# Kernel tuning notes

Hardware: AMD Instinct MI355X
Metric: run time of the kernel (lower is better)

The kernel has to match this reference:

```python
import jax, jax.numpy as jnp
import numpy as np
import math

T = 4096
HID = 2048
H = 16
D = 128
RD = 64            # rotary_dim = head_dim * partial_rotary_factor (0.5)
THETA = 10000.0
EPS = 1e-6
GROUPS = 8
LAYER_IDX = 2
N_LAYERS = 32


def build_slope_tensor(num_heads):
    def get_slopes_power_of_2(n):
        start = 2 ** (-(2 ** (-(math.log2(n) - 3))))
        ratio = start
        return [start * ratio ** i for i in range(n)]
    if math.log2(num_heads).is_integer():
        return get_slopes_power_of_2(num_heads)
    closest = 2 ** math.floor(math.log2(num_heads))
    return (get_slopes_power_of_2(closest)
            + build_slope_tensor(2 * closest)[0::2][: num_heads - closest])


def compute_slope():
    base = np.array(build_slope_tensor(H), dtype=np.float32)
    return jnp.asarray(-base * (1 - (LAYER_IDX - 1) / (N_LAYERS - 1) + 1e-5), dtype=jnp.float32)


def setup_inputs() -> dict:
    key = jax.random.key(0)
    ks = jax.random.split(key, 8)
    s = 0.02
    return {
        "positions": jnp.arange(T, dtype=jnp.int32),
        "hidden_states": jax.random.normal(ks[0], (T, HID), dtype=jnp.float32),
        "recurrent_state": jnp.zeros((1, H, D, D), dtype=jnp.float32),
        "w_qkv": jax.random.normal(ks[1], (HID, 3 * H * D), dtype=jnp.float32) * s,
        "w_g": jax.random.normal(ks[2], (HID, H * D), dtype=jnp.float32) * s,
        "w_dense": jax.random.normal(ks[3], (H * D, HID), dtype=jnp.float32) * s,
        "q_norm_w": jnp.ones((D,), dtype=jnp.float32),
        "k_norm_w": jnp.ones((D,), dtype=jnp.float32),
        "g_norm_w": jnp.ones((H * D,), dtype=jnp.float32),
    }


def _rms(x, w):
    var = jnp.mean(jnp.square(x), axis=-1, keepdims=True)
    return x * jax.lax.rsqrt(var + EPS) * w


def _rope(x, positions):
    # partial neox-style rotary on first RD dims of each head
    inv_freq = 1.0 / (THETA ** (jnp.arange(0, RD, 2, dtype=jnp.float32) / RD))
    freqs = positions.astype(jnp.float32)[:, None] * inv_freq   # [T, RD/2]
    cos = jnp.cos(freqs)[:, None, :]                            # [T, 1, RD/2]
    sin = jnp.sin(freqs)[:, None, :]
    x1 = x[..., : RD // 2]
    x2 = x[..., RD // 2 : RD]
    x_pass = x[..., RD:]
    return jnp.concatenate([x1 * cos - x2 * sin, x2 * cos + x1 * sin, x_pass], axis=-1)


def reference(positions, hidden_states, recurrent_state,
              w_qkv, w_g, w_dense, q_norm_w, k_norm_w, g_norm_w):
    t = hidden_states.shape[0]
    qkv = (hidden_states @ w_qkv).reshape(t, 3, H, D)
    q, k, v = qkv[:, 0], qkv[:, 1], qkv[:, 2]
    q = _rms(q, q_norm_w)
    k = _rms(k, k_norm_w)
    q = _rope(q, positions)
    k = _rope(k, positions)

    slope = compute_slope()                    # [H], negative
    decay = jnp.exp(slope)                     # per-head per-step decay
    scale = D ** -0.5
    q = (q * scale).astype(jnp.float32)
    k = k.astype(jnp.float32)
    v = v.astype(jnp.float32)

    def step(S, qkv_t):
        q_t, k_t, v_t = qkv_t                  # each [H, D]
        S = S * decay[:, None, None] + k_t[:, :, None] * v_t[:, None, :]
        o_t = jnp.einsum('hk,hkv->hv', q_t, S)
        return S, o_t

    S0 = recurrent_state[0].astype(jnp.float32)   # [H, K, V]
    S_final, o = jax.lax.scan(step, S0, (q, k, v))
    attn = o.reshape(t, H * D)

    gate = jax.nn.sigmoid(hidden_states @ w_g)
    # GroupRMSNorm: normalize per group of size (H*D)/GROUPS, scale by full weight
    g = attn.reshape(t, GROUPS, (H * D) // GROUPS)
    var = jnp.mean(jnp.square(g), axis=-1, keepdims=True)
    g = (g * jax.lax.rsqrt(var + EPS)).reshape(t, H * D) * g_norm_w

    out = (g * gate) @ w_dense
    return out, S_final[None]
```

## Files before the change

kernel.cpp:

```cpp
#include <hip/hip_runtime.h>
#include <hip/hip_bf16.h>

using bf16x8 = __attribute__((ext_vector_type(8))) __bf16;
using f32x4  = __attribute__((ext_vector_type(4))) float;

constexpr int T_SEQ = 4096;
constexpr int HID_C = 2048;
constexpr int NH    = 16;
constexpr int QKV_N = 6144;

__device__ __forceinline__ float head_slope(int h) {
    return -exp2f(-0.5f * (float)(h + 1)) * 0.967751935483871f;
}

__device__ __forceinline__ ushort f2bfu(float f) {
    __hip_bfloat16 h = __float2bfloat16(f);
    return *(ushort*)&h;
}
__device__ __forceinline__ float bfu2f(ushort u) {
    union { unsigned int i; float f; } x; x.i = ((unsigned int)u) << 16; return x.f;
}

__device__ __forceinline__ void async16(const ushort* g, ushort* l) {
    __builtin_amdgcn_global_load_lds((const __attribute__((address_space(1))) void*)g,
                                     (__attribute__((address_space(3))) void*)l, 16, 0, 0);
}

template<int N> __device__ __forceinline__ void waitcnt_vm() {
    if constexpr (N == 0)      asm volatile("s_waitcnt vmcnt(0)" ::: "memory");
    else if constexpr (N == 2) asm volatile("s_waitcnt vmcnt(2)" ::: "memory");
    else if constexpr (N == 4) asm volatile("s_waitcnt vmcnt(4)" ::: "memory");
    else if constexpr (N == 6) asm volatile("s_waitcnt vmcnt(6)" ::: "memory");
}

__device__ __forceinline__ void cvt_body(const float* __restrict__ src, ushort* __restrict__ dst,
                                         int bid, int tid) {
    int i = (bid * 256 + tid) * 8;
    float4 a = *(const float4*)(src + i);
    float4 b = *(const float4*)(src + i + 4);
    ushort4 ua = {f2bfu(a.x), f2bfu(a.y), f2bfu(a.z), f2bfu(a.w)};
    ushort4 ub = {f2bfu(b.x), f2bfu(b.y), f2bfu(b.z), f2bfu(b.w)};
    *(ushort4*)(dst + i) = ua;
    *(ushort4*)(dst + i + 4) = ub;
}

__device__ __forceinline__ void transpose_body(const float* __restrict__ src,
                                               ushort* __restrict__ dst,
                                               int R, int C, int bx, int by, int t,
                                               ushort (*tile)[68]) {
    int tr = by * 64, tc = bx * 64;
    int r0 = t >> 4;
    int c4 = (t & 15) << 2;
#pragma unroll
    for (int p = 0; p < 4; ++p) {
        int row = r0 + p * 16;
        float4 v = *(const float4*)&src[(size_t)(tr + row) * C + tc + c4];
        tile[row][c4 + 0] = f2bfu(v.x);
        tile[row][c4 + 1] = f2bfu(v.y);
        tile[row][c4 + 2] = f2bfu(v.z);
        tile[row][c4 + 3] = f2bfu(v.w);
    }
    __syncthreads();
#pragma unroll
    for (int p = 0; p < 4; ++p) {
        int orow = r0 + p * 16;
        ushort4 u;
        u.x = tile[c4 + 0][orow];
        u.y = tile[c4 + 1][orow];
        u.z = tile[c4 + 2][orow];
        u.w = tile[c4 + 3][orow];
        *(ushort4*)&dst[(size_t)(tc + orow) * R + tr + c4] = u;
    }
}

__global__ __launch_bounds__(256) void prep_all(const float* __restrict__ hidden,
                                                ushort* __restrict__ hid_b,
                                                const float* __restrict__ w_qkv,
                                                ushort* __restrict__ wqkv_t,
                                                const float* __restrict__ w_g,
                                                ushort* __restrict__ wg_t,
                                                const float* __restrict__ w_dense,
                                                ushort* __restrict__ wd_t,
                                                const int* __restrict__ positions,
                                                float2* __restrict__ ropet) {
    __shared__ ushort tile[64][68];
    int b = blockIdx.x, t = threadIdx.x;
    if (b < 4096) {
        cvt_body(hidden, hid_b, b, t);
    } else if (b < 7168) {
        int bb = b - 4096;
        transpose_body(w_qkv, wqkv_t, HID_C, QKV_N, bb % 96, bb / 96, t, tile);
    } else if (b < 8192) {
        int bb = b - 7168;
        transpose_body(w_g, wg_t, HID_C, HID_C, bb % 32, bb / 32, t, tile);
    } else if (b < 9216) {
        int bb = b - 8192;
        transpose_body(w_dense, wd_t, HID_C, HID_C, bb % 32, bb / 32, t, tile);
    } else {
        int i = (b - 9216) * 256 + t;
        int tt = i >> 5, fi = i & 31;
        float inv = expf((float)fi * -0.2878231366f);
        float freq = (float)positions[tt] * inv;
        float sn, cs;
        sincosf(freq, &sn, &cs);
        ropet[i] = make_float2(cs, sn);
    }
}

template<int MI, int BN>
__device__ __forceinline__ void gemm8_core(const ushort* __restrict__ Ag,
                                           const ushort* __restrict__ Bg,
                                           int K, int bm, int bn,
                                           ushort* sh, f32x4 (&acc)[MI][4]) {
    constexpr int WM = 16 / MI;
    constexpr int WN = 8 / WM;
    constexpr int SB = BN / 128;
    constexpr int AH = (MI >= 8) ? 2 : 1;
    constexpr int MH = MI / AH;

    const int tid  = threadIdx.x;
    const int lane = tid & 63;
    const int wave = tid >> 6;
    const int lane15 = lane & 15, quad = lane >> 4;
    const int wm = wave / WN, wn = wave % WN;
    const int swz = lane15 & 7;

    ushort* const ldsA0 = sh;
    ushort* const ldsA1 = sh + 16384;
    ushort* const ldsB0 = sh + 32768;
    ushort* const ldsB1 = sh + 32768 + BN * 64;

    const int srow = lane >> 3;
    const int scol = ((lane & 7) ^ srow) << 3;
    const ushort* gA = Ag + (size_t)(bm + srow) * K + scol;
    const ushort* gB = Bg + (size_t)(bn + srow) * K + scol;
    const int ro  = wave * 16;
    const int roB = wave * 8 * SB;
    const int NT = K >> 6;

#define STAGE_A(L, k0) do { \
    _Pragma("unroll") for (int h = 0; h < 2; ++h) \
    _Pragma("unroll") for (int q = 0; q < 2; ++q) \
        async16(gA + (size_t)((h) * 128 + ro + q * 8) * K + (k0), (L) + ((h) * 128 + ro + q * 8) * 64); } while (0)
#define STAGE_B(L, k0) do { \
    _Pragma("unroll") for (int h = 0; h < 2; ++h) \
    _Pragma("unroll") for (int q = 0; q < SB; ++q) \
        async16(gB + (size_t)((h) * (BN / 2) + roB + q * 8) * K + (k0), (L) + ((h) * (BN / 2) + roB + q * 8) * 64); } while (0)

    STAGE_A(ldsA0, 0);
    STAGE_B(ldsB0, 0);
    waitcnt_vm<0>();
    asm volatile("s_barrier" ::: "memory");

    for (int t = 0; t < NT; ++t) {
        const ushort* LA = (t & 1) ? ldsA1 : ldsA0;
        const ushort* LB = (t & 1) ? ldsB1 : ldsB0;
        ushort* LAn = (t & 1) ? ldsA0 : ldsA1;
        ushort* LBn = (t & 1) ? ldsB0 : ldsB1;
        bf16x8 bfr[4][2];
#pragma unroll
        for (int j = 0; j < 4; ++j)
#pragma unroll
            for (int ks = 0; ks < 2; ++ks)
                bfr[j][ks] = *(const bf16x8*)&LB[(wn * 64 + j * 16 + lane15) * 64 + (((ks * 4 + quad) ^ swz) << 3)];
        bf16x8 af0[MH][2];
#pragma unroll
        for (int i = 0; i < MH; ++i)
#pragma unroll
            for (int ks = 0; ks < 2; ++ks)
                af0[i][ks] = *(const bf16x8*)&LA[(wm * (MI * 16) + i * 16 + lane15) * 64 + (((ks * 4 + quad) ^ swz) << 3)];
        if (t + 1 < NT) {
            STAGE_A(LAn, (t + 1) << 6);
            STAGE_B(LBn, (t + 1) << 6);
        }
        __builtin_amdgcn_s_setprio(1);
#pragma unroll
        for (int i = 0; i < MH; ++i)
#pragma unroll
            for (int j = 0; j < 4; ++j)
#pragma unroll
                for (int ks = 0; ks < 2; ++ks)
                    acc[i][j] = __builtin_amdgcn_mfma_f32_16x16x32_bf16(af0[i][ks], bfr[j][ks], acc[i][j], 0, 0, 0);
        __builtin_amdgcn_s_setprio(0);
        if constexpr (AH == 2) {
            bf16x8 af1[MH][2];
#pragma unroll
            for (int i = 0; i < MH; ++i)
#pragma unroll
                for (int ks = 0; ks < 2; ++ks)
                    af1[i][ks] = *(const bf16x8*)&LA[(wm * (MI * 16) + (MH + i) * 16 + lane15) * 64 + (((ks * 4 + quad) ^ swz) << 3)];
            __builtin_amdgcn_s_setprio(1);
#pragma unroll
            for (int i = 0; i < MH; ++i)
#pragma unroll
                for (int j = 0; j < 4; ++j)
#pragma unroll
                    for (int ks = 0; ks < 2; ++ks)
                        acc[MH + i][j] = __builtin_amdgcn_mfma_f32_16x16x32_bf16(af1[i][ks], bfr[j][ks], acc[MH + i][j], 0, 0, 0);
            __builtin_amdgcn_s_setprio(0);
        }
        waitcnt_vm<0>();
        asm volatile("s_barrier" ::: "memory");
    }
#undef STAGE_A
#undef STAGE_B
}

__device__ __forceinline__ void gemm4_core(const ushort* __restrict__ Ag,
                                           const ushort* __restrict__ Bg,
                                           int K, int bm, int bn,
                                           ushort* sh, f32x4 (&acc)[4][4]) {
    const int tid  = threadIdx.x;
    const int lane = tid & 63;
    const int wave = tid >> 6;
    const int lane15 = lane & 15, quad = lane >> 4;
    const int wm = wave >> 1, wn = wave & 1;
    const int swz = lane15 & 7;

    ushort* const ldsA0 = sh;
    ushort* const ldsA1 = sh + 8192;
    ushort* const ldsB0 = sh + 16384;
    ushort* const ldsB1 = sh + 24576;

    const int srow = lane >> 3;
    const int scol = ((lane & 7) ^ srow) << 3;
    const ushort* gA = Ag + (size_t)(bm + srow) * K + scol;
    const ushort* gB = Bg + (size_t)(bn + srow) * K + scol;
    const int ro = wave * 32;
    const int NT = K >> 6;

#define STG(L, g, k0) do { \
    _Pragma("unroll") for (int q = 0; q < 4; ++q) \
        async16((g) + (size_t)(ro + q * 8) * K + (k0), (L) + (ro + q * 8) * 64); } while (0)

    STG(ldsA0, gA, 0);
    STG(ldsB0, gB, 0);
    waitcnt_vm<0>();
    asm volatile("s_barrier" ::: "memory");

    for (int t = 0; t < NT; ++t) {
        const ushort* LA = (t & 1) ? ldsA1 : ldsA0;
        const ushort* LB = (t & 1) ? ldsB1 : ldsB0;
        ushort* LAn = (t & 1) ? ldsA0 : ldsA1;
        ushort* LBn = (t & 1) ? ldsB0 : ldsB1;
        bf16x8 bfr[4][2];
#pragma unroll
        for (int j = 0; j < 4; ++j)
#pragma unroll
            for (int ks = 0; ks < 2; ++ks)
                bfr[j][ks] = *(const bf16x8*)&LB[(wn * 64 + j * 16 + lane15) * 64 + (((ks * 4 + quad) ^ swz) << 3)];
        bf16x8 af[4][2];
#pragma unroll
        for (int i = 0; i < 4; ++i)
#pragma unroll
            for (int ks = 0; ks < 2; ++ks)
                af[i][ks] = *(const bf16x8*)&LA[(wm * 64 + i * 16 + lane15) * 64 + (((ks * 4 + quad) ^ swz) << 3)];
        if (t + 1 < NT) {
            STG(LAn, gA, (t + 1) << 6);
            STG(LBn, gB, (t + 1) << 6);
        }
        __builtin_amdgcn_s_setprio(1);
#pragma unroll
        for (int i = 0; i < 4; ++i)
#pragma unroll
            for (int j = 0; j < 4; ++j)
#pragma unroll
                for (int ks = 0; ks < 2; ++ks)
                    acc[i][j] = __builtin_amdgcn_mfma_f32_16x16x32_bf16(af[i][ks], bfr[j][ks], acc[i][j], 0, 0, 0);
        __builtin_amdgcn_s_setprio(0);
        waitcnt_vm<0>();
        asm volatile("s_barrier" ::: "memory");
    }
#undef STG
}

__global__ __launch_bounds__(512, 2) void gemm_fused(const ushort* __restrict__ A,
                                                     const ushort* __restrict__ Bcat,
                                                     ushort* __restrict__ qkv,
                                                     ushort* __restrict__ gate,
                                                     ushort* __restrict__ kT,
                                                     ushort* __restrict__ vT,
                                                     const float2* __restrict__ tab,
                                                     const float* __restrict__ qw,
                                                     const float* __restrict__ kw, int K) {
    __shared__ ushort sh[65536];
    int bid = blockIdx.x;
    int x = bid & 7, w = bid >> 3;
    int rm = x >> 2, rn = x & 3;
    int wm_i = w >> 3, wn_i = w & 7;
    int bm = (rm * 8 + wm_i) * 256;
    int bn = (rn * 8 + wn_i) * 256;
    f32x4 acc[8][4] = {};
    gemm8_core<8, 256>(A, Bcat, K, bm, bn, sh, acc);

    int lane = threadIdx.x & 63, wave = threadIdx.x >> 6;
    int lane15 = lane & 15, quad = lane >> 4;
    int wm = wave >> 2, wn = wave & 3;
    constexpr int S = 132;

    if (bn < 4096) {
        bool isq = bn < 2048;
        const float* wnorm = isq ? qw : kw;
        int hq = wn >> 1, dl = (wn & 1) * 64;
        int rowbase = bm + wm * 128;
        float w4[4];
#pragma unroll
        for (int j = 0; j < 4; ++j) w4[j] = wnorm[dl + j * 16 + lane15];
        float* ssb = (float*)&sh[63488];
#pragma unroll
        for (int i = 0; i < 8; ++i)
#pragma unroll
            for (int r = 0; r < 4; ++r) {
                float s2 = 0.f;
#pragma unroll
                for (int j = 0; j < 4; ++j) { float xv = acc[i][j][r]; s2 += xv * xv; }
                s2 += __shfl_xor(s2, 1);
                s2 += __shfl_xor(s2, 2);
                s2 += __shfl_xor(s2, 4);
                s2 += __shfl_xor(s2, 8);
                if (lane15 == 0) ssb[wave * 128 + i * 16 + quad * 4 + r] = s2;
            }
        __syncthreads();
        float sc = isq ? 0.08838834764831845f : 1.0f;
#pragma unroll
        for (int i = 0; i < 8; ++i)
#pragma unroll
            for (int r = 0; r < 4; ++r) {
                int row = i * 16 + quad * 4 + r;
                float ssf = ssb[wave * 128 + row] + ssb[(wave ^ 1) * 128 + row];
                float rr = rsqrtf(ssf * (1.0f / 128.0f) + 1e-6f);
                float xx[4];
#pragma unroll
                for (int j = 0; j < 4; ++j) xx[j] = acc[i][j][r] * rr * w4[j];
                if (dl == 0) {
                    int t = rowbase + row;
                    float2 rt0 = tab[t * 32 + lane15];
                    float2 rt1 = tab[t * 32 + 16 + lane15];
                    float a0 = xx[0], b0 = xx[2], a1 = xx[1], b1 = xx[3];
                    xx[0] = a0 * rt0.x - b0 * rt0.y;
                    xx[2] = b0 * rt0.x + a0 * rt0.y;
                    xx[1] = a1 * rt1.x - b1 * rt1.y;
                    xx[3] = b1 * rt1.x + a1 * rt1.y;
                }
#pragma unroll
                for (int j = 0; j < 4; ++j) acc[i][j][r] = xx[j] * sc;
            }
#pragma unroll
        for (int i = 0; i < 8; ++i)
#pragma unroll
            for (int j = 0; j < 4; ++j) {
                int col = bn + wn * 64 + j * 16 + lane15;
#pragma unroll
                for (int r = 0; r < 4; ++r)
                    qkv[(size_t)(rowbase + i * 16 + quad * 4 + r) * QKV_N + col] = f2bfu(acc[i][j][r]);
            }
        if (!isq) {
            ushort* L = sh;
            int h0 = (bn - 2048) >> 7;
            int c0 = bm >> 7;
            __syncthreads();
#pragma unroll
            for (int cq = 0; cq < 2; ++cq) {
                if (wm == cq) {
#pragma unroll
                    for (int i = 0; i < 8; ++i)
#pragma unroll
                        for (int j = 0; j < 4; ++j) {
                            int d_local = dl + j * 16 + lane15;
#pragma unroll
                            for (int r = 0; r < 4; ++r)
                                L[hq * 128 * S + d_local * S + i * 16 + quad * 4 + r] = f2bfu(acc[i][j][r]);
                        }
                }
                __syncthreads();
#pragma unroll
                for (int p = 0; p < 16; ++p) {
                    int lin = (p * 512 + threadIdx.x) * 4;
                    int hq2 = lin >> 14;
                    int wi = lin & 16383;
                    int d = wi >> 7, t4 = wi & 127;
                    const ushort* lp = &L[hq2 * 128 * S + d * S + t4];
                    ushort4 u = { lp[0], lp[1], lp[2], lp[3] };
                    *(ushort4*)&kT[((size_t)((h0 + hq2) * 32 + c0 + cq) * 128 + d) * 128 + t4] = u;
                }
                __syncthreads();
            }
        }
        return;
    }

    if (bn < QKV_N) {
        ushort* L = sh;
        int h0 = (bn - 4096) >> 7;
        int c0 = bm >> 7;
        int hq = wn >> 1;
        int dl = (wn & 1) * 64;
#pragma unroll
        for (int cq = 0; cq < 2; ++cq) {
            if (wm == cq) {
#pragma unroll
                for (int i = 0; i < 8; ++i)
#pragma unroll
                    for (int j = 0; j < 4; ++j) {
                        int d_local = dl + j * 16 + lane15;
#pragma unroll
                        for (int r = 0; r < 4; ++r)
                            L[hq * 128 * S + d_local * S + i * 16 + quad * 4 + r] = f2bfu(acc[i][j][r]);
                    }
            }
            __syncthreads();
#pragma unroll
            for (int p = 0; p < 16; ++p) {
                int lin = (p * 512 + threadIdx.x) * 4;
                int hq2 = lin >> 14;
                int wi = lin & 16383;
                int d = wi >> 7, t4 = wi & 127;
                const ushort* lp = &L[hq2 * 128 * S + d * S + t4];
                ushort4 u = { lp[0], lp[1], lp[2], lp[3] };
                *(ushort4*)&vT[((size_t)((h0 + hq2) * 32 + c0 + cq) * 128 + d) * 128 + t4] = u;
            }
            __syncthreads();
        }
        return;
    }

    int cb = (bn - QKV_N) + wn * 64;
    int rb = bm + wm * 128;
#pragma unroll
    for (int i = 0; i < 8; ++i)
#pragma unroll
        for (int j = 0; j < 4; ++j) {
            int col = cb + j * 16 + lane15;
#pragma unroll
            for (int r = 0; r < 4; ++r) {
                float v = 1.0f / (1.0f + __expf(-acc[i][j][r]));
                gate[(size_t)(rb + i * 16 + quad * 4 + r) * HID_C + col] = f2bfu(v);
            }
        }
}

__global__ __launch_bounds__(256, 2) void gemm_dense(const ushort* __restrict__ A,
                                                     const ushort* __restrict__ Bt,
                                                     float* __restrict__ Cout, int N, int K) {
    __shared__ ushort sh[32768];
    int bid = blockIdx.x;
    int x = bid & 7, w = bid >> 3;
    int rm = x >> 1, rn = x & 1;
    int wm_i = w >> 3, wn_i = w & 7;
    int bm = (rm * 8 + wm_i) * 128;
    int bn = (rn * 8 + wn_i) * 128;
    f32x4 acc[4][4] = {};
    gemm4_core(A, Bt, K, bm, bn, sh, acc);

    int lane = threadIdx.x & 63, wave = threadIdx.x >> 6;
    int lane15 = lane & 15, quad = lane >> 4;
    int wm = wave >> 1, wn = wave & 1;
    int cb = bn + wn * 64;
    int rb = bm + wm * 64;
#pragma unroll
    for (int i = 0; i < 4; ++i)
#pragma unroll
        for (int j = 0; j < 4; ++j) {
            int col = cb + j * 16 + lane15;
#pragma unroll
            for (int r = 0; r < 4; ++r)
                Cout[(size_t)(rb + i * 16 + quad * 4 + r) * N + col] = acc[i][j][r];
        }
}

__global__ __launch_bounds__(256) void chunk_partial(const ushort* __restrict__ kT,
                                                     const ushort* __restrict__ vT,
                                                     ushort* __restrict__ PT) {
    int c = blockIdx.x, h = blockIdx.y;
    float slope = head_slope(h);
    float lam_inv = __expf(-slope);
    int tid = threadIdx.x, lane = tid & 63, wave = tid >> 6;
    int lane15 = lane & 15, quad = lane >> 4;
    int wv = (wave & 1) * 64, wd = (wave >> 1) * 64;
    const ushort* vbase = vT + ((size_t)(h * 32 + c) * 128) * 128;
    const ushort* kbase = kT + ((size_t)(h * 32 + c) * 128) * 128;
    f32x4 acc[4][4] = {};
#pragma unroll
    for (int j0 = 0; j0 < 128; j0 += 32) {
        float w8[8];
        w8[0] = __expf(slope * (float)(127 - (j0 + quad * 8)));
#pragma unroll
        for (int kk = 1; kk < 8; ++kk) w8[kk] = w8[kk - 1] * lam_inv;
        bf16x8 afr[4], bfr[4];
#pragma unroll
        for (int i = 0; i < 4; ++i) {
            bf16x8 v = *(const bf16x8*)&vbase[(size_t)(wv + i * 16 + lane15) * 128 + j0 + quad * 8];
#pragma unroll
            for (int kk = 0; kk < 8; ++kk) afr[i][kk] = (__bf16)((float)v[kk] * w8[kk]);
        }
#pragma unroll
        for (int j = 0; j < 4; ++j)
            bfr[j] = *(const bf16x8*)&kbase[(size_t)(wd + j * 16 + lane15) * 128 + j0 + quad * 8];
#pragma unroll
        for (int i = 0; i < 4; ++i)
#pragma unroll
            for (int j = 0; j < 4; ++j)
                acc[i][j] = __builtin_amdgcn_mfma_f32_16x16x32_bf16(afr[i], bfr[j], acc[i][j], 0, 0, 0);
    }
    ushort* out = PT + ((size_t)c * 16 + h) * 16384;
#pragma unroll
    for (int i = 0; i < 4; ++i)
#pragma unroll
        for (int j = 0; j < 4; ++j)
#pragma unroll
            for (int r = 0; r < 4; ++r)
                out[(size_t)(wv + i * 16 + quad * 4 + r) * 128 + wd + j * 16 + lane15] = f2bfu(acc[i][j][r]);
}

__global__ __launch_bounds__(128) void scan_states(const ushort* __restrict__ PT,
                                                   const float* __restrict__ S0,
                                                   ushort* __restrict__ Spb,
                                                   float* __restrict__ Sfin) {
    int hv = blockIdx.x;
    int d = threadIdx.x;
    int h = hv >> 7, v = hv & 127;
    float lamC = __expf(head_slope(h) * 128.0f);
    float s = S0[(size_t)h * 16384 + d * 128 + v];
#pragma unroll
    for (int c = 0; c < 32; ++c) {
        size_t idx = ((size_t)c * 2048 + hv) * 128 + d;
        Spb[idx] = f2bfu(s);
        s = s * lamC + bfu2f(PT[idx]);
    }
    Sfin[(size_t)h * 16384 + d * 128 + v] = s;
}

__global__ __launch_bounds__(256) void chunk_out(const ushort* __restrict__ qkv,
                                                 const ushort* __restrict__ vT,
                                                 const ushort* __restrict__ Spb,
                                                 ushort* __restrict__ o) {
    int c = blockIdx.x, h = blockIdx.y;
    float slope = head_slope(h);
    __shared__ ushort Ps[128 * 136];
    int tid = threadIdx.x, lane = tid & 63, wave = tid >> 6;
    int lane15 = lane & 15, quad = lane >> 4;
    int t0 = c * 128;
    int tt0 = wave, tt1 = 7 - wave;
    const ushort* qbase = qkv + (size_t)t0 * QKV_N + h * 128;
    const ushort* kbase = qbase + 2048;

    bf16x8 qf0[4], qf1[4];
#pragma unroll
    for (int ds = 0; ds < 4; ++ds) {
        qf0[ds] = *(const bf16x8*)&qbase[(size_t)(tt0 * 16 + lane15) * QKV_N + ds * 32 + quad * 8];
        qf1[ds] = *(const bf16x8*)&qbase[(size_t)(tt1 * 16 + lane15) * QKV_N + ds * 32 + quad * 8];
    }
    f32x4 s0a[4] = {};
    f32x4 s1a[8] = {};
#pragma unroll
    for (int st = 0; st < 8; ++st) {
        if (st <= tt1) {
            bf16x8 kf[4];
#pragma unroll
            for (int ds = 0; ds < 4; ++ds)
                kf[ds] = *(const bf16x8*)&kbase[(size_t)(st * 16 + lane15) * QKV_N + ds * 32 + quad * 8];
#pragma unroll
            for (int ds = 0; ds < 4; ++ds)
                s1a[st] = __builtin_amdgcn_mfma_f32_16x16x32_bf16(qf1[ds], kf[ds], s1a[st], 0, 0, 0);
            if (st <= tt0) {
#pragma unroll
                for (int ds = 0; ds < 4; ++ds)
                    s0a[st] = __builtin_amdgcn_mfma_f32_16x16x32_bf16(qf0[ds], kf[ds], s0a[st], 0, 0, 0);
            }
        }
    }
    int stmax0 = tt0 + ((tt0 & 1) ? 0 : 1);
    int stmax1 = tt1 + ((tt1 & 1) ? 0 : 1);
#pragma unroll
    for (int st = 0; st < 8; ++st) {
        if (st <= stmax1) {
#pragma unroll
            for (int r = 0; r < 4; ++r) {
                int t = tt1 * 16 + quad * 4 + r;
                int s = st * 16 + lane15;
                float val = 0.f;
                if (st <= tt1) val = (s <= t) ? s1a[st][r] * __expf(slope * (float)(t - s)) : 0.f;
                Ps[t * 136 + s] = f2bfu(val);
            }
        }
    }
#pragma unroll
    for (int st = 0; st < 5; ++st) {
        if (st <= stmax0) {
#pragma unroll
            for (int r = 0; r < 4; ++r) {
                int t = tt0 * 16 + quad * 4 + r;
                int s = st * 16 + lane15;
                float val = 0.f;
                if (st <= tt0) val = (s <= t) ? s0a[st][r] * __expf(slope * (float)(t - s)) : 0.f;
                Ps[t * 136 + s] = f2bfu(val);
            }
        }
    }
    __syncthreads();
    f32x4 oa0[8] = {};
    f32x4 oa1[8] = {};
    float lam0 = __expf(slope * (float)(tt0 * 16 + lane15 + 1));
    float lam1 = __expf(slope * (float)(tt1 * 16 + lane15 + 1));
    bf16x8 qs0[4], qs1[4];
#pragma unroll
    for (int ds = 0; ds < 4; ++ds)
#pragma unroll
        for (int kk = 0; kk < 8; ++kk) {
            qs0[ds][kk] = (__bf16)((float)qf0[ds][kk] * lam0);
            qs1[ds][kk] = (__bf16)((float)qf1[ds][kk] * lam1);
        }
    const ushort* spb = Spb + ((size_t)c * 2048 + h * 128) * 128;
#pragma unroll
    for (int vt = 0; vt < 8; ++vt)
#pragma unroll
        for (int ds = 0; ds < 4; ++ds) {
            bf16x8 bfrag = *(const bf16x8*)&spb[(vt * 16 + lane15) * 128 + ds * 32 + quad * 8];
            oa0[vt] = __builtin_amdgcn_mfma_f32_16x16x32_bf16(qs0[ds], bfrag, oa0[vt], 0, 0, 0);
            oa1[vt] = __builtin_amdgcn_mfma_f32_16x16x32_bf16(qs1[ds], bfrag, oa1[vt], 0, 0, 0);
        }
    const ushort* vbase = vT + ((size_t)(h * 32 + c) * 128) * 128;
    int ns0 = (tt0 + 2) >> 1, ns1 = (tt1 + 2) >> 1;
#pragma unroll
    for (int s32 = 0; s32 < 4; ++s32) {
        if (s32 < ns1) {
            bf16x8 af = *(const bf16x8*)&Ps[(tt1 * 16 + lane15) * 136 + s32 * 32 + quad * 8];
#pragma unroll
            for (int vt = 0; vt < 8; ++vt) {
                bf16x8 bfrag = *(const bf16x8*)&vbase[(size_t)(vt * 16 + lane15) * 128 + s32 * 32 + quad * 8];
                oa1[vt] = __builtin_amdgcn_mfma_f32_16x16x32_bf16(af, bfrag, oa1[vt], 0, 0, 0);
            }
        }
    }
#pragma unroll
    for (int s32 = 0; s32 < 2; ++s32) {
        if (s32 < ns0) {
            bf16x8 af = *(const bf16x8*)&Ps[(tt0 * 16 + lane15) * 136 + s32 * 32 + quad * 8];
#pragma unroll
            for (int vt = 0; vt < 8; ++vt) {
                bf16x8 bfrag = *(const bf16x8*)&vbase[(size_t)(vt * 16 + lane15) * 128 + s32 * 32 + quad * 8];
                oa0[vt] = __builtin_amdgcn_mfma_f32_16x16x32_bf16(af, bfrag, oa0[vt], 0, 0, 0);
            }
        }
    }
#pragma unroll
    for (int vt = 0; vt < 8; ++vt)
#pragma unroll
        for (int r = 0; r < 4; ++r) {
            o[(size_t)(t0 + tt0 * 16 + quad * 4 + r) * 2048 + h * 128 + vt * 16 + lane15] = f2bfu(oa0[vt][r]);
            o[(size_t)(t0 + tt1 * 16 + quad * 4 + r) * 2048 + h * 128 + vt * 16 + lane15] = f2bfu(oa1[vt][r]);
        }
}

__global__ __launch_bounds__(256) void gnorm_gate(const ushort* __restrict__ o,
                                                  const ushort* __restrict__ gate,
                                                  const float* __restrict__ gw,
                                                  ushort* __restrict__ gg) {
    int t = blockIdx.x;
    int tid = threadIdx.x;
    const ushort* op = o + (size_t)t * 2048 + tid * 8;
    bf16x8 xv = *(const bf16x8*)op;
    float x[8];
    float ss = 0.0f;
#pragma unroll
    for (int i = 0; i < 8; ++i) { x[i] = (float)xv[i]; ss += x[i] * x[i]; }
#pragma unroll
    for (int off = 16; off > 0; off >>= 1) ss += __shfl_xor(ss, off);
    float r = rsqrtf(ss * (1.0f / 256.0f) + 1e-6f);
    const ushort* gp = gate + (size_t)t * 2048;
#pragma unroll
    for (int i = 0; i < 8; ++i) {
        int j = tid * 8 + i;
        float val = x[i] * r * gw[j] * bfu2f(gp[j]);
        gg[(size_t)t * 2048 + j] = f2bfu(val);
    }
}

extern "C" void kernel_launch(void* const* d_in, const int* in_sizes, int n_in,
                              void* d_out, int out_size, void* d_ws, size_t ws_size,
                              hipStream_t stream) {
    const int* positions   = (const int*)d_in[0];
    const float* hidden    = (const float*)d_in[1];
    const float* S0        = (const float*)d_in[2];
    const float* w_qkv     = (const float*)d_in[3];
    const float* w_g       = (const float*)d_in[4];
    const float* w_dense   = (const float*)d_in[5];
    const float* qw        = (const float*)d_in[6];
    const float* kw        = (const float*)d_in[7];
    const float* gw        = (const float*)d_in[8];

    char* ws = (char*)d_ws;
    ushort* qkv     = (ushort*)ws;
    ushort* wqkv_t  = (ushort*)(ws + 50331648);
    ushort* wg_t    = (ushort*)(ws + 75497472);
    float2* ropet   = (float2*)(ws + 159383552);
    ushort* PT      = (ushort*)(ws + 50331648);
    ushort* wd_t    = (ushort*)(ws + 83886080);
    ushort* gatebuf = (ushort*)(ws + 92274688);
    ushort* hid_b   = (ushort*)(ws + 109051904);
    ushort* Spb     = (ushort*)(ws + 109051904);
    ushort* kT      = (ushort*)(ws + 125829120);
    ushort* vT      = (ushort*)(ws + 142606336);
    ushort* gg      = (ushort*)ws;

    float* out  = (float*)d_out;
    float* Sfin = out + (size_t)T_SEQ * HID_C;
    ushort* obuf = (ushort*)d_out;

    prep_all<<<9728, 256, 0, stream>>>(hidden, hid_b, w_qkv, wqkv_t, w_g, wg_t,
                                       w_dense, wd_t, positions, ropet);

    gemm_fused<<<dim3(512), 512, 0, stream>>>(hid_b, wqkv_t, qkv, gatebuf, kT, vT,
                                              ropet, qw, kw, HID_C);

    chunk_partial<<<dim3(32, 16), 256, 0, stream>>>(kT, vT, PT);
    scan_states<<<2048, 128, 0, stream>>>(PT, S0, Spb, Sfin);
    chunk_out<<<dim3(32, 16), 256, 0, stream>>>(qkv, vT, Spb, obuf);
    gnorm_gate<<<T_SEQ, 256, 0, stream>>>(obuf, gatebuf, gw, gg);

    gemm_dense<<<dim3(512), 256, 0, stream>>>(gg, wd_t, out, HID_C, HID_C);
}
```

Before: 409.6 us.

## Remap fused QKV/gate GEMM waves to 64x128 tiles so each wave owns full heads

The fused QKV+gate GEMM changes its per-wave tile from 128 rows x 64 columns to 64 rows x 128 columns (4x2 wave grid). Each wave now covers a whole 128-wide head, so the Q/K RMSNorm reduction stays inside the wave and the LDS exchange of partial sums plus a block barrier go away. The epilogue and the K/V transpose staging are re-indexed to match. The LDS read mix per k-step also shifts toward more B-fragment loads and fewer A-fragment loads.

```diff
diff --git a/kernel.cpp b/kernel.cpp
--- a/kernel.cpp
+++ b/kernel.cpp
@@ -107,48 +107,36 @@
     }
 }
 
-template<int MI, int BN>
-__device__ __forceinline__ void gemm8_core(const ushort* __restrict__ Ag,
-                                           const ushort* __restrict__ Bg,
-                                           int K, int bm, int bn,
-                                           ushort* sh, f32x4 (&acc)[MI][4]) {
-    constexpr int WM = 16 / MI;
-    constexpr int WN = 8 / WM;
-    constexpr int SB = BN / 128;
-    constexpr int AH = (MI >= 8) ? 2 : 1;
-    constexpr int MH = MI / AH;
-
+__device__ __forceinline__ void gemm8w_core(const ushort* __restrict__ Ag,
+                                            const ushort* __restrict__ Bg,
+                                            int K, int bm, int bn,
+                                            ushort* sh, f32x4 (&acc)[4][8]) {
     const int tid  = threadIdx.x;
     const int lane = tid & 63;
     const int wave = tid >> 6;
     const int lane15 = lane & 15, quad = lane >> 4;
-    const int wm = wave / WN, wn = wave % WN;
+    const int wm = wave >> 1, wn = wave & 1;
     const int swz = lane15 & 7;
 
     ushort* const ldsA0 = sh;
     ushort* const ldsA1 = sh + 16384;
     ushort* const ldsB0 = sh + 32768;
-    ushort* const ldsB1 = sh + 32768 + BN * 64;
+    ushort* const ldsB1 = sh + 49152;
 
     const int srow = lane >> 3;
     const int scol = ((lane & 7) ^ srow) << 3;
     const ushort* gA = Ag + (size_t)(bm + srow) * K + scol;
     const ushort* gB = Bg + (size_t)(bn + srow) * K + scol;
-    const int ro  = wave * 16;
-    const int roB = wave * 8 * SB;
+    const int ro = wave * 16;
     const int NT = K >> 6;
 
-#define STAGE_A(L, k0) do { \
+#define STAGE8(L, g, k0) do { \
     _Pragma("unroll") for (int h = 0; h < 2; ++h) \
     _Pragma("unroll") for (int q = 0; q < 2; ++q) \
-        async16(gA + (size_t)((h) * 128 + ro + q * 8) * K + (k0), (L) + ((h) * 128 + ro + q * 8) * 64); } while (0)
-#define STAGE_B(L, k0) do { \
-    _Pragma("unroll") for (int h = 0; h < 2; ++h) \
-    _Pragma("unroll") for (int q = 0; q < SB; ++q) \
-        async16(gB + (size_t)((h) * (BN / 2) + roB + q * 8) * K + (k0), (L) + ((h) * (BN / 2) + roB + q * 8) * 64); } while (0)
-
-    STAGE_A(ldsA0, 0);
-    STAGE_B(ldsB0, 0);
+        async16((g) + (size_t)((h) * 128 + ro + q * 8) * K + (k0), (L) + ((h) * 128 + ro + q * 8) * 64); } while (0)
+
+    STAGE8(ldsA0, gA, 0);
+    STAGE8(ldsB0, gB, 0);
     waitcnt_vm<0>();
     asm volatile("s_barrier" ::: "memory");
 
@@ -157,53 +145,50 @@
         const ushort* LB = (t & 1) ? ldsB1 : ldsB0;
         ushort* LAn = (t & 1) ? ldsA0 : ldsA1;
         ushort* LBn = (t & 1) ? ldsB0 : ldsB1;
-        bf16x8 bfr[4][2];
+        bf16x8 af[4][2];
+#pragma unroll
+        for (int i = 0; i < 4; ++i)
+#pragma unroll
+            for (int ks = 0; ks < 2; ++ks)
+                af[i][ks] = *(const bf16x8*)&LA[(wm * 64 + i * 16 + lane15) * 64 + (((ks * 4 + quad) ^ swz) << 3)];
+        bf16x8 bf0[4][2];
 #pragma unroll
         for (int j = 0; j < 4; ++j)
 #pragma unroll
             for (int ks = 0; ks < 2; ++ks)
-                bfr[j][ks] = *(const bf16x8*)&LB[(wn * 64 + j * 16 + lane15) * 64 + (((ks * 4 + quad) ^ swz) << 3)];
-        bf16x8 af0[MH][2];
-#pragma unroll
-        for (int i = 0; i < MH; ++i)
+                bf0[j][ks] = *(const bf16x8*)&LB[(wn * 128 + j * 16 + lane15) * 64 + (((ks * 4 + quad) ^ swz) << 3)];
+        if (t + 1 < NT) {
+            STAGE8(LAn, gA, (t + 1) << 6);
+            STAGE8(LBn, gB, (t + 1) << 6);
+        }
+        __builtin_amdgcn_s_setprio(1);
+#pragma unroll
+        for (int i = 0; i < 4; ++i)
+#pragma unroll
+            for (int j = 0; j < 4; ++j)
+#pragma unroll
+                for (int ks = 0; ks < 2; ++ks)
+                    acc[i][j] = __builtin_amdgcn_mfma_f32_16x16x32_bf16(af[i][ks], bf0[j][ks], acc[i][j], 0, 0, 0);
+        __builtin_amdgcn_s_setprio(0);
+        bf16x8 bf1[4][2];
+#pragma unroll
+        for (int j = 0; j < 4; ++j)
 #pragma unroll
             for (int ks = 0; ks < 2; ++ks)
-                af0[i][ks] = *(const bf16x8*)&LA[(wm * (MI * 16) + i * 16 + lane15) * 64 + (((ks * 4 + quad) ^ swz) << 3)];
-        if (t + 1 < NT) {
-            STAGE_A(LAn, (t + 1) << 6);
-            STAGE_B(LBn, (t + 1) << 6);
-        }
+                bf1[j][ks] = *(const bf16x8*)&LB[(wn * 128 + (4 + j) * 16 + lane15) * 64 + (((ks * 4 + quad) ^ swz) << 3)];
         __builtin_amdgcn_s_setprio(1);
 #pragma unroll
-        for (int i = 0; i < MH; ++i)
+        for (int i = 0; i < 4; ++i)
 #pragma unroll
             for (int j = 0; j < 4; ++j)
 #pragma unroll
                 for (int ks = 0; ks < 2; ++ks)
-                    acc[i][j] = __builtin_amdgcn_mfma_f32_16x16x32_bf16(af0[i][ks], bfr[j][ks], acc[i][j], 0, 0, 0);
+                    acc[i][4 + j] = __builtin_amdgcn_mfma_f32_16x16x32_bf16(af[i][ks], bf1[j][ks], acc[i][4 + j], 0, 0, 0);
         __builtin_amdgcn_s_setprio(0);
-        if constexpr (AH == 2) {
-            bf16x8 af1[MH][2];
-#pragma unroll
-            for (int i = 0; i < MH; ++i)
-#pragma unroll
-                for (int ks = 0; ks < 2; ++ks)
-                    af1[i][ks] = *(const bf16x8*)&LA[(wm * (MI * 16) + (MH + i) * 16 + lane15) * 64 + (((ks * 4 + quad) ^ swz) << 3)];
-            __builtin_amdgcn_s_setprio(1);
-#pragma unroll
-            for (int i = 0; i < MH; ++i)
-#pragma unroll
-                for (int j = 0; j < 4; ++j)
-#pragma unroll
-                    for (int ks = 0; ks < 2; ++ks)
-                        acc[MH + i][j] = __builtin_amdgcn_mfma_f32_16x16x32_bf16(af1[i][ks], bfr[j][ks], acc[MH + i][j], 0, 0, 0);
-            __builtin_amdgcn_s_setprio(0);
-        }
         waitcnt_vm<0>();
         asm volatile("s_barrier" ::: "memory");
     }
-#undef STAGE_A
-#undef STAGE_B
+#undef STAGE8
 }
 
 __device__ __forceinline__ void gemm4_core(const ushort* __restrict__ Ag,
@@ -290,66 +275,53 @@
     int wm_i = w >> 3, wn_i = w & 7;
     int bm = (rm * 8 + wm_i) * 256;
     int bn = (rn * 8 + wn_i) * 256;
-    f32x4 acc[8][4] = {};
-    gemm8_core<8, 256>(A, Bcat, K, bm, bn, sh, acc);
+    f32x4 acc[4][8] = {};
+    gemm8w_core(A, Bcat, K, bm, bn, sh, acc);
 
     int lane = threadIdx.x & 63, wave = threadIdx.x >> 6;
     int lane15 = lane & 15, quad = lane >> 4;
-    int wm = wave >> 2, wn = wave & 3;
+    int wm = wave >> 1, wn = wave & 1;
     constexpr int S = 132;
 
     if (bn < 4096) {
         bool isq = bn < 2048;
         const float* wnorm = isq ? qw : kw;
-        int hq = wn >> 1, dl = (wn & 1) * 64;
-        int rowbase = bm + wm * 128;
-        float w4[4];
-#pragma unroll
-        for (int j = 0; j < 4; ++j) w4[j] = wnorm[dl + j * 16 + lane15];
-        float* ssb = (float*)&sh[63488];
-#pragma unroll
-        for (int i = 0; i < 8; ++i)
+        float w8a[8];
+#pragma unroll
+        for (int j = 0; j < 8; ++j) w8a[j] = wnorm[j * 16 + lane15];
+        float sc = isq ? 0.08838834764831845f : 1.0f;
+        int rowbase = bm + wm * 64;
+#pragma unroll
+        for (int i = 0; i < 4; ++i)
 #pragma unroll
             for (int r = 0; r < 4; ++r) {
                 float s2 = 0.f;
 #pragma unroll
-                for (int j = 0; j < 4; ++j) { float xv = acc[i][j][r]; s2 += xv * xv; }
+                for (int j = 0; j < 8; ++j) { float xv = acc[i][j][r]; s2 += xv * xv; }
                 s2 += __shfl_xor(s2, 1);
                 s2 += __shfl_xor(s2, 2);
                 s2 += __shfl_xor(s2, 4);
                 s2 += __shfl_xor(s2, 8);
-                if (lane15 == 0) ssb[wave * 128 + i * 16 + quad * 4 + r] = s2;
-            }
-        __syncthreads();
-        float sc = isq ? 0.08838834764831845f : 1.0f;
-#pragma unroll
-        for (int i = 0; i < 8; ++i)
-#pragma unroll
-            for (int r = 0; r < 4; ++r) {
-                int row = i * 16 + quad * 4 + r;
-                float ssf = ssb[wave * 128 + row] + ssb[(wave ^ 1) * 128 + row];
-                float rr = rsqrtf(ssf * (1.0f / 128.0f) + 1e-6f);
-                float xx[4];
-#pragma unroll
-                for (int j = 0; j < 4; ++j) xx[j] = acc[i][j][r] * rr * w4[j];
-                if (dl == 0) {
-                    int t = rowbase + row;
-                    float2 rt0 = tab[t * 32 + lane15];
-                    float2 rt1 = tab[t * 32 + 16 + lane15];
-                    float a0 = xx[0], b0 = xx[2], a1 = xx[1], b1 = xx[3];
-                    xx[0] = a0 * rt0.x - b0 * rt0.y;
-                    xx[2] = b0 * rt0.x + a0 * rt0.y;
-                    xx[1] = a1 * rt1.x - b1 * rt1.y;
-                    xx[3] = b1 * rt1.x + a1 * rt1.y;
-                }
-#pragma unroll
-                for (int j = 0; j < 4; ++j) acc[i][j][r] = xx[j] * sc;
-            }
-#pragma unroll
-        for (int i = 0; i < 8; ++i)
-#pragma unroll
-            for (int j = 0; j < 4; ++j) {
-                int col = bn + wn * 64 + j * 16 + lane15;
+                float rr = rsqrtf(s2 * (1.0f / 128.0f) + 1e-6f);
+                float xx[8];
+#pragma unroll
+                for (int j = 0; j < 8; ++j) xx[j] = acc[i][j][r] * rr * w8a[j];
+                int t = rowbase + i * 16 + quad * 4 + r;
+                float2 rt0 = tab[t * 32 + lane15];
+                float2 rt1 = tab[t * 32 + 16 + lane15];
+                float a0 = xx[0], b0 = xx[2], a1 = xx[1], b1 = xx[3];
+                xx[0] = a0 * rt0.x - b0 * rt0.y;
+                xx[2] = b0 * rt0.x + a0 * rt0.y;
+                xx[1] = a1 * rt1.x - b1 * rt1.y;
+                xx[3] = b1 * rt1.x + a1 * rt1.y;
+#pragma unroll
+                for (int j = 0; j < 8; ++j) acc[i][j][r] = xx[j] * sc;
+            }
+#pragma unroll
+        for (int i = 0; i < 4; ++i)
+#pragma unroll
+            for (int j = 0; j < 8; ++j) {
+                int col = bn + wn * 128 + j * 16 + lane15;
 #pragma unroll
                 for (int r = 0; r < 4; ++r)
                     qkv[(size_t)(rowbase + i * 16 + quad * 4 + r) * QKV_N + col] = f2bfu(acc[i][j][r]);
@@ -358,18 +330,19 @@
             ushort* L = sh;
             int h0 = (bn - 2048) >> 7;
             int c0 = bm >> 7;
-            __syncthreads();
 #pragma unroll
             for (int cq = 0; cq < 2; ++cq) {
-                if (wm == cq) {
-#pragma unroll
-                    for (int i = 0; i < 8; ++i)
-#pragma unroll
-                        for (int j = 0; j < 4; ++j) {
-                            int d_local = dl + j * 16 + lane15;
-#pragma unroll
-                            for (int r = 0; r < 4; ++r)
-                                L[hq * 128 * S + d_local * S + i * 16 + quad * 4 + r] = f2bfu(acc[i][j][r]);
+                if ((wm >> 1) == cq) {
+#pragma unroll
+                    for (int i = 0; i < 4; ++i)
+#pragma unroll
+                        for (int j = 0; j < 8; ++j) {
+                            int d_local = j * 16 + lane15;
+#pragma unroll
+                            for (int r = 0; r < 4; ++r) {
+                                int t_local = (wm & 1) * 64 + i * 16 + quad * 4 + r;
+                                L[wn * 128 * S + d_local * S + t_local] = f2bfu(acc[i][j][r]);
+                            }
                         }
                 }
                 __syncthreads();
@@ -393,19 +366,19 @@
         ushort* L = sh;
         int h0 = (bn - 4096) >> 7;
         int c0 = bm >> 7;
-        int hq = wn >> 1;
-        int dl = (wn & 1) * 64;
 #pragma unroll
         for (int cq = 0; cq < 2; ++cq) {
-            if (wm == cq) {
-#pragma unroll
-                for (int i = 0; i < 8; ++i)
-#pragma unroll
-                    for (int j = 0; j < 4; ++j) {
-                        int d_local = dl + j * 16 + lane15;
-#pragma unroll
-                        for (int r = 0; r < 4; ++r)
-                            L[hq * 128 * S + d_local * S + i * 16 + quad * 4 + r] = f2bfu(acc[i][j][r]);
+            if ((wm >> 1) == cq) {
+#pragma unroll
+                for (int i = 0; i < 4; ++i)
+#pragma unroll
+                    for (int j = 0; j < 8; ++j) {
+                        int d_local = j * 16 + lane15;
+#pragma unroll
+                        for (int r = 0; r < 4; ++r) {
+                            int t_local = (wm & 1) * 64 + i * 16 + quad * 4 + r;
+                            L[wn * 128 * S + d_local * S + t_local] = f2bfu(acc[i][j][r]);
+                        }
                     }
             }
             __syncthreads();
@@ -424,12 +397,12 @@
         return;
     }
 
-    int cb = (bn - QKV_N) + wn * 64;
-    int rb = bm + wm * 128;
-#pragma unroll
-    for (int i = 0; i < 8; ++i)
-#pragma unroll
-        for (int j = 0; j < 4; ++j) {
+    int cb = (bn - QKV_N) + wn * 128;
+    int rb = bm + wm * 64;
+#pragma unroll
+    for (int i = 0; i < 4; ++i)
+#pragma unroll
+        for (int j = 0; j < 8; ++j) {
             int col = cb + j * 16 + lane15;
 #pragma unroll
             for (int r = 0; r < 4; ++r) {
```

Measured after the change: 389.0 us. 1.05x faster.
